# Kernel tuning notes

Measured on AMD Instinct MI355X. Metric: run time of the kernel, lower is better.

Reference implementation:

```python
import jax, jax.numpy as jnp
import numpy as np

N_EMBD = 1024
N_HEAD = 16
HEAD_SIZE = N_EMBD // N_HEAD
EPS = 1e-5


def layer_norm(x, gamma, beta):
    mu = jnp.mean(x, axis=-1, keepdims=True)
    var = jnp.var(x, axis=-1, keepdims=True)
    return (x - mu) * jax.lax.rsqrt(var + EPS) * gamma + beta


def setup_inputs() -> dict:
    key = jax.random.key(0)
    ks = jax.random.split(key, 12)
    B, T, C, H, hs = 2, 2048, N_EMBD, N_HEAD, HEAD_SIZE
    s = lambda fan_in: 1.0 / np.sqrt(fan_in)
    return {
        "x": jax.random.normal(ks[0], (B, T, C), dtype=jnp.float32),
        "Wq": jax.random.normal(ks[1], (H, C, hs), dtype=jnp.float32) * s(C),
        "Wk": jax.random.normal(ks[2], (H, C, hs), dtype=jnp.float32) * s(C),
        "Wv": jax.random.normal(ks[3], (H, C, hs), dtype=jnp.float32) * s(C),
        "Wproj": jax.random.normal(ks[4], (C, C), dtype=jnp.float32) * s(C),
        "bproj": jax.random.normal(ks[5], (C,), dtype=jnp.float32) * 0.01,
        "g1": jnp.ones((C,), dtype=jnp.float32),
        "b1": jnp.zeros((C,), dtype=jnp.float32),
        "g2": jnp.ones((C,), dtype=jnp.float32),
        "b2": jnp.zeros((C,), dtype=jnp.float32),
        "W_ff1": jax.random.normal(ks[6], (C, 4 * C), dtype=jnp.float32) * s(C),
        "b_ff1": jax.random.normal(ks[7], (4 * C,), dtype=jnp.float32) * 0.01,
        "W_ff2": jax.random.normal(ks[8], (4 * C, C), dtype=jnp.float32) * s(4 * C),
        "b_ff2": jax.random.normal(ks[9], (C,), dtype=jnp.float32) * 0.01,
    }


def reference(x, Wq, Wk, Wv, Wproj, bproj, g1, b1, g2, b2, W_ff1, b_ff1, W_ff2, b_ff2):
    B, T, C = x.shape
    # --- LN1 + multi-head causal self-attention ---
    h = layer_norm(x, g1, b1)
    q = jnp.einsum("btc,hcd->bhtd", h, Wq)  # [B,H,T,hs]
    k = jnp.einsum("btc,hcd->bhtd", h, Wk)
    v = jnp.einsum("btc,hcd->bhtd", h, Wv)
    scale = HEAD_SIZE ** -0.5
    wei = jnp.einsum("bhtd,bhsd->bhts", q, k) * scale  # [B,H,T,T]
    mask = jnp.tril(jnp.ones((T, T), dtype=bool))
    wei = jnp.where(mask, wei, -jnp.inf)
    wei = jax.nn.softmax(wei, axis=-1)
    out = jnp.einsum("bhts,bhsd->bhtd", wei, v)  # [B,H,T,hs]
    out = out.transpose(0, 2, 1, 3).reshape(B, T, C)  # concat heads
    sa = out @ Wproj + bproj
    x = x + sa
    # --- LN2 + FFN ---
    h2 = layer_norm(x, g2, b2)
    ff = jax.nn.relu(h2 @ W_ff1 + b_ff1) @ W_ff2 + b_ff2
    return x + ff
```

## Files before the change

### kernel.cpp

```cpp
#include <hip/hip_runtime.h>
#include <hip/hip_bf16.h>

#define N_EMBD 1024
#define N_HEAD 16
#define HEADSZ 64
#define BATCH  2
#define SEQ    2048
#define ROWS   (BATCH*SEQ)

typedef __attribute__((ext_vector_type(8))) short bf16x8;
typedef __attribute__((ext_vector_type(4))) float f32x4;

__device__ __forceinline__ short f2bs(float v){
    union { __hip_bfloat16 b; short s; } u; u.b = __float2bfloat16(v); return u.s;
}
__device__ __forceinline__ short scale8th(short s){
    union { unsigned i; float f; } u; u.i = ((unsigned)(unsigned short)s) << 16;
    return f2bs(u.f * 0.125f);
}
__device__ __forceinline__ void gload16(const short* g, short* l){
    __builtin_amdgcn_global_load_lds(
        (const __attribute__((address_space(1))) unsigned int*)g,
        (__attribute__((address_space(3))) unsigned int*)l, 16, 0, 0);
}

__global__ __launch_bounds__(256) void tr_cvt(const float* __restrict__ in,
                                              short* __restrict__ out,
                                              int R, int Cc,
                                              size_t in_z, size_t out_z)
{
    __shared__ float t[32][33];
    const int tx = threadIdx.x & 31, ty = threadIdx.x >> 5;
    const int j0 = blockIdx.x * 32, i0 = blockIdx.y * 32;
    const float* ip = in + (size_t)blockIdx.z * in_z;
    short* op = out + (size_t)blockIdx.z * out_z;
#pragma unroll
    for (int p = 0; p < 4; ++p)
        t[ty + p * 8][tx] = ip[(size_t)(i0 + ty + p * 8) * Cc + j0 + tx];
    __syncthreads();
#pragma unroll
    for (int p = 0; p < 4; ++p)
        op[(size_t)(j0 + ty + p * 8) * R + i0 + tx] = f2bs(t[tx][ty + p * 8]);
}

__global__ __launch_bounds__(256) void tr3_cvt(const float* __restrict__ Wq,
                                               const float* __restrict__ Wk,
                                               const float* __restrict__ Wv,
                                               short* __restrict__ w2t)
{
    __shared__ float t[32][33];
    const int tx = threadIdx.x & 31, ty = threadIdx.x >> 5;
    const int which = blockIdx.z >> 4, head = blockIdx.z & 15;
    const int j0 = blockIdx.x * 32, i0 = blockIdx.y * 32;
    const float* ip = (which == 0 ? Wq : which == 1 ? Wk : Wv) + (size_t)head * 65536;
    short* op = w2t + (size_t)which * 1048576 + (size_t)head * 65536;
#pragma unroll
    for (int p = 0; p < 4; ++p)
        t[ty + p * 8][tx] = ip[(size_t)(i0 + ty + p * 8) * 64 + j0 + tx];
    __syncthreads();
#pragma unroll
    for (int p = 0; p < 4; ++p)
        op[(size_t)(j0 + ty + p * 8) * 1024 + i0 + tx] = f2bs(t[tx][ty + p * 8]);
}

__global__ __launch_bounds__(256) void vt_tr(const short* __restrict__ qkv,
                                             short* __restrict__ vt)
{
    __shared__ short t[64][65];
    const int tid = threadIdx.x;
    const int sr = tid >> 2, sc = (tid & 3) * 16;
    const int col0 = blockIdx.x * 64, tok0 = blockIdx.y * 64;
    const short* ip = qkv + (size_t)(tok0 + sr) * 3072 + 2048 + col0 + sc;
    bf16x8 v0 = *(const bf16x8*)ip;
    bf16x8 v1 = *(const bf16x8*)(ip + 8);
#pragma unroll
    for (int i = 0; i < 8; ++i) { t[sr][sc + i] = v0[i]; t[sr][sc + 8 + i] = v1[i]; }
    __syncthreads();
    bf16x8 a, bq;
#pragma unroll
    for (int i = 0; i < 8; ++i) { a[i] = t[sc + i][sr]; bq[i] = t[sc + 8 + i][sr]; }
    short* op = vt + (size_t)(col0 + sr) * 4096 + tok0 + sc;
    *(bf16x8*)op = a;
    *(bf16x8*)(op + 8) = bq;
}

__global__ __launch_bounds__(256) void ln_k(const float* __restrict__ x,
                                            const float* __restrict__ g,
                                            const float* __restrict__ bta,
                                            short* __restrict__ out)
{
    const int row = blockIdx.x;
    const int tid = threadIdx.x;
    const float* xr = x + (size_t)row * N_EMBD;
    float4 v = *(const float4*)(xr + tid * 4);
    float s  = v.x + v.y + v.z + v.w;
    float s2 = v.x * v.x + v.y * v.y + v.z * v.z + v.w * v.w;
#pragma unroll
    for (int off = 32; off; off >>= 1) {
        s  += __shfl_xor(s,  off, 64);
        s2 += __shfl_xor(s2, off, 64);
    }
    __shared__ float rs[4], rs2[4];
    const int wave = tid >> 6, lane = tid & 63;
    if (lane == 0) { rs[wave] = s; rs2[wave] = s2; }
    __syncthreads();
    s  = rs[0] + rs[1] + rs[2] + rs[3];
    s2 = rs2[0] + rs2[1] + rs2[2] + rs2[3];
    const float mean = s * (1.f / N_EMBD);
    const float var  = s2 * (1.f / N_EMBD) - mean * mean;
    const float rsig = rsqrtf(var + 1e-5f);
    float4 gv = *(const float4*)(g + tid * 4);
    float4 bv = *(const float4*)(bta + tid * 4);
    short4 o;
    o.x = f2bs((v.x - mean) * rsig * gv.x + bv.x);
    o.y = f2bs((v.y - mean) * rsig * gv.y + bv.y);
    o.z = f2bs((v.z - mean) * rsig * gv.z + bv.z);
    o.w = f2bs((v.w - mean) * rsig * gv.w + bv.w);
    *(short4*)(out + (size_t)row * N_EMBD + tid * 4) = o;
}

__global__ __launch_bounds__(256) void pln_fin(const float* __restrict__ p0,
                                               const float* __restrict__ p1,
                                               const float* __restrict__ bias,
                                               const float* __restrict__ x,
                                               const float* __restrict__ g,
                                               const float* __restrict__ bta,
                                               float* __restrict__ x2,
                                               short* __restrict__ h2)
{
    const int row = blockIdx.x, tid = threadIdx.x;
    const size_t base = (size_t)row * N_EMBD + tid * 4;
    float4 a  = *(const float4*)(p0 + base);
    float4 c  = *(const float4*)(p1 + base);
    float4 xx = *(const float4*)(x + base);
    float4 bb = *(const float4*)(bias + tid * 4);
    float4 v;
    v.x = a.x + c.x + xx.x + bb.x;
    v.y = a.y + c.y + xx.y + bb.y;
    v.z = a.z + c.z + xx.z + bb.z;
    v.w = a.w + c.w + xx.w + bb.w;
    *(float4*)(x2 + base) = v;
    float s  = v.x + v.y + v.z + v.w;
    float s2 = v.x * v.x + v.y * v.y + v.z * v.z + v.w * v.w;
#pragma unroll
    for (int off = 32; off; off >>= 1) {
        s  += __shfl_xor(s,  off, 64);
        s2 += __shfl_xor(s2, off, 64);
    }
    __shared__ float rs[4], rs2[4];
    const int wave = tid >> 6, lane = tid & 63;
    if (lane == 0) { rs[wave] = s; rs2[wave] = s2; }
    __syncthreads();
    s  = rs[0] + rs[1] + rs[2] + rs[3];
    s2 = rs2[0] + rs2[1] + rs2[2] + rs2[3];
    const float mean = s * (1.f / N_EMBD);
    const float var  = s2 * (1.f / N_EMBD) - mean * mean;
    const float rsig = rsqrtf(var + 1e-5f);
    float4 gv = *(const float4*)(g + tid * 4);
    float4 bv = *(const float4*)(bta + tid * 4);
    short4 o;
    o.x = f2bs((v.x - mean) * rsig * gv.x + bv.x);
    o.y = f2bs((v.y - mean) * rsig * gv.y + bv.y);
    o.z = f2bs((v.z - mean) * rsig * gv.z + bv.z);
    o.w = f2bs((v.w - mean) * rsig * gv.w + bv.w);
    *(short4*)(h2 + base) = o;
}

__global__ __launch_bounds__(256) void mfma_gemm(
    const short* __restrict__ A,
    const short* __restrict__ Bt,
    const float* __restrict__ bias,
    const float* __restrict__ resid,
    float* __restrict__ outf,
    float* __restrict__ outf2,
    short* __restrict__ outb,
    int M, int N, int K, int kz, int relu)
{
    __shared__ __align__(16) short As[128 * 32];
    __shared__ __align__(16) short Bs[128 * 32];
    const int tid  = threadIdx.x;
    const int lane = tid & 63, w = tid >> 6;
    const int quad = lane >> 4, l16 = lane & 15;
    const int row0 = blockIdx.y * 128, col0 = blockIdx.x * 128;
    const int wm = (w >> 1) * 64, wn = (w & 1) * 64;
    const int koff = blockIdx.z * kz;
    const int kend = kz ? kz : K;

    f32x4 acc[4][4];
#pragma unroll
    for (int i = 0; i < 4; ++i)
#pragma unroll
        for (int j = 0; j < 4; ++j)
            acc[i][j] = f32x4{0.f, 0.f, 0.f, 0.f};

    const int c0  = w * 128 + lane;
    const int c1  = c0 + 64;
    const int ar0 = c0 >> 2, ak0 = (((c0 & 3) ^ ((ar0 >> 1) & 3))) * 8;
    const int ar1 = c1 >> 2, ak1 = (((c1 & 3) ^ ((ar1 >> 1) & 3))) * 8;
    const short* aG0 = A  + (size_t)(row0 + ar0) * K + koff + ak0;
    const short* aG1 = A  + (size_t)(row0 + ar1) * K + koff + ak1;
    const short* bG0 = Bt + (size_t)(col0 + ar0) * K + koff + ak0;
    const short* bG1 = Bt + (size_t)(col0 + ar1) * K + koff + ak1;
    short* aL0 = As + (size_t)w * 1024;
    short* aL1 = aL0 + 512;
    short* bL0 = Bs + (size_t)w * 1024;
    short* bL1 = bL0 + 512;

    const int gsw = (quad ^ ((l16 >> 1) & 3)) * 8;

    for (int k0 = 0; k0 < kend; k0 += 32) {
        __syncthreads();
        gload16(aG0 + k0, aL0);
        gload16(aG1 + k0, aL1);
        gload16(bG0 + k0, bL0);
        gload16(bG1 + k0, bL1);
        asm volatile("s_waitcnt vmcnt(0)" ::: "memory");
        __syncthreads();

        bf16x8 af[4], bfr[4];
#pragma unroll
        for (int i = 0; i < 4; ++i)
            af[i]  = *(const bf16x8*)(As + (wm + i * 16 + l16) * 32 + gsw);
#pragma unroll
        for (int j = 0; j < 4; ++j)
            bfr[j] = *(const bf16x8*)(Bs + (wn + j * 16 + l16) * 32 + gsw);
#pragma unroll
        for (int i = 0; i < 4; ++i)
#pragma unroll
            for (int j = 0; j < 4; ++j)
                acc[i][j] = __builtin_amdgcn_mfma_f32_16x16x32_bf16(
                    af[i], bfr[j], acc[i][j], 0, 0, 0);
    }

    float* of = blockIdx.z ? outf2 : outf;
#pragma unroll
    for (int i = 0; i < 4; ++i) {
        const int rbase = row0 + wm + i * 16 + quad * 4;
#pragma unroll
        for (int j = 0; j < 4; ++j) {
            const int c = col0 + wn + j * 16 + l16;
            const float bv = bias ? bias[c] : 0.f;
#pragma unroll
            for (int r = 0; r < 4; ++r) {
                float v = acc[i][j][r] + bv;
                if (relu) v = fmaxf(v, 0.f);
                const size_t idx = (size_t)(rbase + r) * N + c;
                if (resid) v += resid[idx];
                if (outb) outb[idx] = f2bs(v);
                else      of[idx] = v;
            }
        }
    }
}

__global__ __launch_bounds__(256) void mfma_gemm64(
    const short* __restrict__ A,
    const short* __restrict__ Bt,
    float* __restrict__ outf,
    float* __restrict__ outf2,
    int K, int kz)
{
    __shared__ __align__(16) short As[64 * 32];
    __shared__ __align__(16) short Bs[128 * 32];
    const int tid  = threadIdx.x;
    const int lane = tid & 63, w = tid >> 6;
    const int quad = lane >> 4, l16 = lane & 15;
    const int lin  = (int)blockIdx.y * 8 + (int)blockIdx.x;
    const int swz  = (lin & 7) * 64 + (lin >> 3);
    const int col0 = (swz & 7) * 128;
    const int row0 = (swz >> 3) * 64;
    const int wr = w >> 1, wc = w & 1;
    const int koff = blockIdx.z * kz;

    f32x4 acc[2][4];
#pragma unroll
    for (int i = 0; i < 2; ++i)
#pragma unroll
        for (int j = 0; j < 4; ++j)
            acc[i][j] = f32x4{0.f, 0.f, 0.f, 0.f};

    const int ia  = w * 64 + lane;
    const int ar  = ia >> 2;
    const int aak = ((ia & 3) ^ ((ar >> 1) & 3)) * 8;
    const short* aG = A + (size_t)(row0 + ar) * K + koff + aak;
    short* aL = As + w * 512;
    const int c0  = w * 128 + lane;
    const int c1  = c0 + 64;
    const int br0 = c0 >> 2, bk0 = ((c0 & 3) ^ ((br0 >> 1) & 3)) * 8;
    const int br1 = c1 >> 2, bk1 = ((c1 & 3) ^ ((br1 >> 1) & 3)) * 8;
    const short* bG0 = Bt + (size_t)(col0 + br0) * K + koff + bk0;
    const short* bG1 = Bt + (size_t)(col0 + br1) * K + koff + bk1;
    short* bL0 = Bs + (size_t)w * 1024;
    short* bL1 = bL0 + 512;

    const int gsw = (quad ^ ((l16 >> 1) & 3)) * 8;

    for (int k0 = 0; k0 < kz; k0 += 32) {
        __syncthreads();
        gload16(aG + k0, aL);
        gload16(bG0 + k0, bL0);
        gload16(bG1 + k0, bL1);
        asm volatile("s_waitcnt vmcnt(0)" ::: "memory");
        __syncthreads();

        bf16x8 af[2], bfr[4];
#pragma unroll
        for (int i = 0; i < 2; ++i)
            af[i]  = *(const bf16x8*)(As + (wr * 32 + i * 16 + l16) * 32 + gsw);
#pragma unroll
        for (int j = 0; j < 4; ++j)
            bfr[j] = *(const bf16x8*)(Bs + (wc * 64 + j * 16 + l16) * 32 + gsw);
#pragma unroll
        for (int i = 0; i < 2; ++i)
#pragma unroll
            for (int j = 0; j < 4; ++j)
                acc[i][j] = __builtin_amdgcn_mfma_f32_16x16x32_bf16(
                    af[i], bfr[j], acc[i][j], 0, 0, 0);
    }

    float* of = blockIdx.z ? outf2 : outf;
#pragma unroll
    for (int i = 0; i < 2; ++i) {
        const int rbase = row0 + wr * 32 + i * 16 + quad * 4;
#pragma unroll
        for (int j = 0; j < 4; ++j) {
            const int c = col0 + wc * 64 + j * 16 + l16;
#pragma unroll
            for (int r = 0; r < 4; ++r)
                of[(size_t)(rbase + r) * 1024 + c] = acc[i][j][r];
        }
    }
}

__global__ __launch_bounds__(256) void ff2_fin(const float* __restrict__ p0,
                                               const float* __restrict__ bias,
                                               const float* __restrict__ x2,
                                               float* __restrict__ out)
{
    const size_t i = ((size_t)blockIdx.x * 256 + threadIdx.x) * 4;
    float4 a = *(const float4*)(p0 + i);
    float4 b = *(const float4*)(out + i);
    float4 r = *(const float4*)(x2 + i);
    float4 bb = *(const float4*)(bias + (i & 1023));
    float4 o;
    o.x = a.x + b.x + r.x + bb.x;
    o.y = a.y + b.y + r.y + bb.y;
    o.z = a.z + b.z + r.z + bb.z;
    o.w = a.w + b.w + r.w + bb.w;
    *(float4*)(out + i) = o;
}

__global__ __launch_bounds__(256) void attn_k(const short* __restrict__ qkv,
                                              const short* __restrict__ vt,
                                              short* __restrict__ att)
{
    __shared__ __align__(16) short Ks[2][64 * 64];
    __shared__ __align__(16) short Vs[2][64 * 64];
    __shared__ __align__(16) short Ps[64 * 64];
    const int tid  = threadIdx.x;
    const int lane = tid & 63, w = tid >> 6;
    const int quad = lane >> 4, l16 = lane & 15;
    const int bh = blockIdx.y, b = bh >> 4, head = bh & 15;

    const int srow = lane >> 3;
    const int sw   = ((lane & 7) ^ srow) * 8;
    const int cidx = (quad ^ (l16 & 7)) * 8;

    const int k4 = (bh >> 3) & 3;
    int qt = (k4 & 2) ? ((int)blockIdx.x ^ 16) : (int)blockIdx.x;
    if (k4 & 1) qt = 31 - qt;
    const int t0 = qt * 64;
    const int ntiles = qt + 1;

    const short* qp = qkv + (size_t)(b * SEQ + t0 + w * 16 + l16) * 3072
                      + head * 64 + quad * 8;
    bf16x8 qf0 = *(const bf16x8*)qp;
    bf16x8 qf1 = *(const bf16x8*)(qp + 32);
#pragma unroll
    for (int i = 0; i < 8; ++i) { qf0[i] = scale8th(qf0[i]); qf1[i] = scale8th(qf1[i]); }

    float mrow = -INFINITY, lrow = 0.f;
    f32x4 O[4];
#pragma unroll
    for (int jn = 0; jn < 4; ++jn) O[jn] = f32x4{0.f, 0.f, 0.f, 0.f};

    {
        const short* kg = qkv + (size_t)(b * SEQ + w * 16 + srow) * 3072
                          + 1024 + head * 64 + sw;
        const short* vg = vt + (size_t)(head * 64 + w * 16 + srow) * 4096
                          + b * SEQ + sw;
        short* kL = Ks[0] + w * 1024;
        short* vL = Vs[0] + w * 1024;
        gload16(kg, kL); gload16(kg + (size_t)8 * 3072, kL + 512);
        gload16(vg, vL); gload16(vg + (size_t)8 * 4096, vL + 512);
    }

    for (int kt = 0; kt < ntiles; ++kt) {
        const int cur = kt & 1;
        asm volatile("s_waitcnt vmcnt(0) lgkmcnt(0)\n\ts_barrier" ::: "memory");
        if (kt + 1 < ntiles) {
            const int s1 = (kt + 1) * 64;
            const short* kg = qkv + (size_t)(b * SEQ + s1 + w * 16 + srow) * 3072
                              + 1024 + head * 64 + sw;
            const short* vg = vt + (size_t)(head * 64 + w * 16 + srow) * 4096
                              + b * SEQ + s1 + sw;
            short* kL = Ks[cur ^ 1] + w * 1024;
            short* vL = Vs[cur ^ 1] + w * 1024;
            gload16(kg, kL); gload16(kg + (size_t)8 * 3072, kL + 512);
            gload16(vg, vL); gload16(vg + (size_t)8 * 4096, vL + 512);
        }

        f32x4 S[4];
        const short* Kb = Ks[cur];
#pragma unroll
        for (int jn = 0; jn < 4; ++jn) {
            S[jn] = f32x4{0.f, 0.f, 0.f, 0.f};
            const short* kp = Kb + (jn * 16 + l16) * 64;
            bf16x8 b0 = *(const bf16x8*)(kp + cidx);
            bf16x8 b1 = *(const bf16x8*)(kp + (cidx ^ 32));
            S[jn] = __builtin_amdgcn_mfma_f32_16x16x32_bf16(b0, qf0, S[jn], 0, 0, 0);
            S[jn] = __builtin_amdgcn_mfma_f32_16x16x32_bf16(b1, qf1, S[jn], 0, 0, 0);
        }

        float Sv[4][4];
        const int qrow = t0 + w * 16 + l16;
        const int s0 = kt * 64;
#pragma unroll
        for (int jn = 0; jn < 4; ++jn)
#pragma unroll
            for (int r = 0; r < 4; ++r)
                Sv[jn][r] = S[jn][r];
        if (kt == ntiles - 1) {
#pragma unroll
            for (int jn = 0; jn < 4; ++jn)
#pragma unroll
                for (int r = 0; r < 4; ++r)
                    if (s0 + jn * 16 + quad * 4 + r > qrow) Sv[jn][r] = -INFINITY;
        }
        float tmx[4];
#pragma unroll
        for (int jn = 0; jn < 4; ++jn)
            tmx[jn] = fmaxf(fmaxf(Sv[jn][0], Sv[jn][1]), fmaxf(Sv[jn][2], Sv[jn][3]));
        float pm = fmaxf(fmaxf(tmx[0], tmx[1]), fmaxf(tmx[2], tmx[3]));
        pm = fmaxf(pm, __shfl_xor(pm, 16, 64));
        pm = fmaxf(pm, __shfl_xor(pm, 32, 64));
        const float mn    = fmaxf(mrow, pm);
        const float alpha = __expf(mrow - mn);
#pragma unroll
        for (int jn = 0; jn < 4; ++jn)
#pragma unroll
            for (int r = 0; r < 4; ++r)
                Sv[jn][r] = __expf(Sv[jn][r] - mn);
        float tsm[4];
#pragma unroll
        for (int jn = 0; jn < 4; ++jn)
            tsm[jn] = (Sv[jn][0] + Sv[jn][1]) + (Sv[jn][2] + Sv[jn][3]);
        float ps = (tsm[0] + tsm[1]) + (tsm[2] + tsm[3]);
        ps += __shfl_xor(ps, 16, 64);
        ps += __shfl_xor(ps, 32, 64);
        lrow = lrow * alpha + ps;
        mrow = mn;
#pragma unroll
        for (int r = 0; r < 4; ++r) {
            const float a = __shfl(alpha, quad * 4 + r, 64);
#pragma unroll
            for (int jn = 0; jn < 4; ++jn) O[jn][r] *= a;
        }

#pragma unroll
        for (int jn = 0; jn < 4; ++jn) {
            short4 pv;
            pv.x = f2bs(Sv[jn][0]); pv.y = f2bs(Sv[jn][1]);
            pv.z = f2bs(Sv[jn][2]); pv.w = f2bs(Sv[jn][3]);
            const int prow = w * 16 + l16;
            const int pcol = jn * 16 + quad * 4;
            const int chunk = (pcol >> 3) ^ (l16 & 7);
            *(short4*)(Ps + prow * 64 + chunk * 8 + (pcol & 7)) = pv;
        }
        asm volatile("s_waitcnt lgkmcnt(0)" ::: "memory");

        const short* pp = Ps + (w * 16 + l16) * 64;
        bf16x8 pf0 = *(const bf16x8*)(pp + cidx);
        bf16x8 pf1 = *(const bf16x8*)(pp + (cidx ^ 32));
        const short* Vb = Vs[cur];
#pragma unroll
        for (int jn = 0; jn < 4; ++jn) {
            const short* vp = Vb + (jn * 16 + l16) * 64;
            bf16x8 v0 = *(const bf16x8*)(vp + cidx);
            bf16x8 v1 = *(const bf16x8*)(vp + (cidx ^ 32));
            O[jn] = __builtin_amdgcn_mfma_f32_16x16x32_bf16(pf0, v0, O[jn], 0, 0, 0);
            O[jn] = __builtin_amdgcn_mfma_f32_16x16x32_bf16(pf1, v1, O[jn], 0, 0, 0);
        }
    }

#pragma unroll
    for (int r = 0; r < 4; ++r) {
        const float lr  = __shfl(lrow, quad * 4 + r, 64);
        const float inv = 1.f / lr;
        const size_t rowoff = (size_t)(b * SEQ + t0 + w * 16 + quad * 4 + r) * N_EMBD
                              + head * 64 + l16;
#pragma unroll
        for (int jn = 0; jn < 4; ++jn)
            att[rowoff + jn * 16] = f2bs(O[jn][r] * inv);
    }
}

extern "C" void kernel_launch(void* const* d_in, const int* in_sizes, int n_in,
                              void* d_out, int out_size, void* d_ws, size_t ws_size,
                              hipStream_t stream)
{
    const float* x     = (const float*)d_in[0];
    const float* Wq    = (const float*)d_in[1];
    const float* Wk    = (const float*)d_in[2];
    const float* Wv    = (const float*)d_in[3];
    const float* Wproj = (const float*)d_in[4];
    const float* bproj = (const float*)d_in[5];
    const float* g1    = (const float*)d_in[6];
    const float* b1    = (const float*)d_in[7];
    const float* g2    = (const float*)d_in[8];
    const float* b2    = (const float*)d_in[9];
    const float* Wff1  = (const float*)d_in[10];
    const float* bff1  = (const float*)d_in[11];
    const float* Wff2  = (const float*)d_in[12];
    const float* bff2  = (const float*)d_in[13];
    float* out = (float*)d_out;

    char* ws = (char*)d_ws;
    short* w2t  = (short*)(ws + 0);
    short* wpt  = (short*)(ws + 6291456);
    short* wf1t = (short*)(ws + 8388608);
    short* wf2t = (short*)(ws + 16777216);
    short* h    = (short*)(ws + 25165824);
    short* qkv  = (short*)(ws + 33554432);
    short* vt   = (short*)(ws + 58720256);
    short* att  = (short*)(ws + 67108864);
    float* x2   = (float*)(ws + 75497472);
    short* h2   = h;
    float* p0p  = (float*)(ws + 33554432);
    float* p1p  = (float*)(ws + 50331648);
    short* ff   = qkv;
    float* p0f  = (float*)(ws + 0);

    tr3_cvt<<<dim3(2, 32, 48),  256, 0, stream>>>(Wq, Wk, Wv, w2t);
    tr_cvt<<<dim3(32, 32, 1),  256, 0, stream>>>(Wproj, wpt,  1024, 1024, 0, 0);
    tr_cvt<<<dim3(128, 32, 1), 256, 0, stream>>>(Wff1, wf1t,  1024, 4096, 0, 0);
    tr_cvt<<<dim3(32, 128, 1), 256, 0, stream>>>(Wff2, wf2t,  4096, 1024, 0, 0);

    ln_k<<<ROWS, 256, 0, stream>>>(x, g1, b1, h);
    mfma_gemm<<<dim3(3072 / 128, ROWS / 128), 256, 0, stream>>>(
        h, w2t, nullptr, nullptr, nullptr, nullptr, qkv, ROWS, 3072, N_EMBD, 0, 0);
    vt_tr<<<dim3(16, 64), 256, 0, stream>>>(qkv, vt);
    attn_k<<<dim3(32, BATCH * N_HEAD), 256, 0, stream>>>(qkv, vt, att);
    mfma_gemm64<<<dim3(8, 64, 2), 256, 0, stream>>>(att, wpt, p0p, p1p, N_EMBD, 512);
    pln_fin<<<ROWS, 256, 0, stream>>>(p0p, p1p, bproj, x, g2, b2, x2, h2);
    mfma_gemm<<<dim3(4096 / 128, ROWS / 128), 256, 0, stream>>>(
        h2, wf1t, bff1, nullptr, nullptr, nullptr, ff, ROWS, 4096, N_EMBD, 0, 1);
    mfma_gemm64<<<dim3(8, 64, 2), 256, 0, stream>>>(ff, wf2t, p0f, out, 4096, 2048);
    ff2_fin<<<ROWS * N_EMBD / 1024, 256, 0, stream>>>(p0f, bff2, x2, out);
}
```

Baseline: 389.8 us.

## Double-buffer LDS tiles in MFMA GEMM kernels to overlap loads with compute

Both GEMM kernels now keep two LDS buffers for the A and B tiles and issue the global-to-LDS loads for the next K-step before computing on the current one. This replaces the old load-wait-compute sequence that had two barriers per iteration with a single wait and barrier after compute. The aim is to hide global memory latency behind the MFMA work. In exchange, LDS use per block doubles, which may reduce occupancy.

```diff
diff --git a/kernel.cpp b/kernel.cpp
--- a/kernel.cpp
+++ b/kernel.cpp
@@ -176,8 +176,8 @@
     short* __restrict__ outb,
     int M, int N, int K, int kz, int relu)
 {
-    __shared__ __align__(16) short As[128 * 32];
-    __shared__ __align__(16) short Bs[128 * 32];
+    __shared__ __align__(16) short As[2][128 * 32];
+    __shared__ __align__(16) short Bs[2][128 * 32];
     const int tid  = threadIdx.x;
     const int lane = tid & 63, w = tid >> 6;
     const int quad = lane >> 4, l16 = lane & 15;
@@ -201,35 +201,43 @@
     const short* aG1 = A  + (size_t)(row0 + ar1) * K + koff + ak1;
     const short* bG0 = Bt + (size_t)(col0 + ar0) * K + koff + ak0;
     const short* bG1 = Bt + (size_t)(col0 + ar1) * K + koff + ak1;
-    short* aL0 = As + (size_t)w * 1024;
-    short* aL1 = aL0 + 512;
-    short* bL0 = Bs + (size_t)w * 1024;
-    short* bL1 = bL0 + 512;
+    const int lofs = w * 1024;
 
     const int gsw = (quad ^ ((l16 >> 1) & 3)) * 8;
 
+    gload16(aG0, As[0] + lofs);
+    gload16(aG1, As[0] + lofs + 512);
+    gload16(bG0, Bs[0] + lofs);
+    gload16(bG1, Bs[0] + lofs + 512);
+    asm volatile("s_waitcnt vmcnt(0)" ::: "memory");
+    __syncthreads();
+
     for (int k0 = 0; k0 < kend; k0 += 32) {
-        __syncthreads();
-        gload16(aG0 + k0, aL0);
-        gload16(aG1 + k0, aL1);
-        gload16(bG0 + k0, bL0);
-        gload16(bG1 + k0, bL1);
-        asm volatile("s_waitcnt vmcnt(0)" ::: "memory");
-        __syncthreads();
+        const int cur = (k0 >> 5) & 1;
+        if (k0 + 32 < kend) {
+            const int nxt = cur ^ 1;
+            gload16(aG0 + k0 + 32, As[nxt] + lofs);
+            gload16(aG1 + k0 + 32, As[nxt] + lofs + 512);
+            gload16(bG0 + k0 + 32, Bs[nxt] + lofs);
+            gload16(bG1 + k0 + 32, Bs[nxt] + lofs + 512);
+        }
 
         bf16x8 af[4], bfr[4];
 #pragma unroll
         for (int i = 0; i < 4; ++i)
-            af[i]  = *(const bf16x8*)(As + (wm + i * 16 + l16) * 32 + gsw);
+            af[i]  = *(const bf16x8*)(As[cur] + (wm + i * 16 + l16) * 32 + gsw);
 #pragma unroll
         for (int j = 0; j < 4; ++j)
-            bfr[j] = *(const bf16x8*)(Bs + (wn + j * 16 + l16) * 32 + gsw);
+            bfr[j] = *(const bf16x8*)(Bs[cur] + (wn + j * 16 + l16) * 32 + gsw);
 #pragma unroll
         for (int i = 0; i < 4; ++i)
 #pragma unroll
             for (int j = 0; j < 4; ++j)
                 acc[i][j] = __builtin_amdgcn_mfma_f32_16x16x32_bf16(
                     af[i], bfr[j], acc[i][j], 0, 0, 0);
+
+        asm volatile("s_waitcnt vmcnt(0)" ::: "memory");
+        __syncthreads();
     }
 
     float* of = blockIdx.z ? outf2 : outf;
@@ -260,8 +268,8 @@
     float* __restrict__ outf2,
     int K, int kz)
 {
-    __shared__ __align__(16) short As[64 * 32];
-    __shared__ __align__(16) short Bs[128 * 32];
+    __shared__ __align__(16) short As[2][64 * 32];
+    __shared__ __align__(16) short Bs[2][128 * 32];
     const int tid  = threadIdx.x;
     const int lane = tid & 63, w = tid >> 6;
     const int quad = lane >> 4, l16 = lane & 15;
@@ -283,39 +291,48 @@
     const int ar  = ia >> 2;
     const int aak = ((ia & 3) ^ ((ar >> 1) & 3)) * 8;
     const short* aG = A + (size_t)(row0 + ar) * K + koff + aak;
-    short* aL = As + w * 512;
+    const int aofs = w * 512;
     const int c0  = w * 128 + lane;
     const int c1  = c0 + 64;
     const int br0 = c0 >> 2, bk0 = ((c0 & 3) ^ ((br0 >> 1) & 3)) * 8;
     const int br1 = c1 >> 2, bk1 = ((c1 & 3) ^ ((br1 >> 1) & 3)) * 8;
     const short* bG0 = Bt + (size_t)(col0 + br0) * K + koff + bk0;
     const short* bG1 = Bt + (size_t)(col0 + br1) * K + koff + bk1;
-    short* bL0 = Bs + (size_t)w * 1024;
-    short* bL1 = bL0 + 512;
+    const int bofs = w * 1024;
 
     const int gsw = (quad ^ ((l16 >> 1) & 3)) * 8;
 
+    gload16(aG, As[0] + aofs);
+    gload16(bG0, Bs[0] + bofs);
+    gload16(bG1, Bs[0] + bofs + 512);
+    asm volatile("s_waitcnt vmcnt(0)" ::: "memory");
+    __syncthreads();
+
     for (int k0 = 0; k0 < kz; k0 += 32) {
-        __syncthreads();
-        gload16(aG + k0, aL);
-        gload16(bG0 + k0, bL0);
-        gload16(bG1 + k0, bL1);
-        asm volatile("s_waitcnt vmcnt(0)" ::: "memory");
-        __syncthreads();
+        const int cur = (k0 >> 5) & 1;
+        if (k0 + 32 < kz) {
+            const int nxt = cur ^ 1;
+            gload16(aG + k0 + 32, As[nxt] + aofs);
+            gload16(bG0 + k0 + 32, Bs[nxt] + bofs);
+            gload16(bG1 + k0 + 32, Bs[nxt] + bofs + 512);
+        }
 
         bf16x8 af[2], bfr[4];
 #pragma unroll
         for (int i = 0; i < 2; ++i)
-            af[i]  = *(const bf16x8*)(As + (wr * 32 + i * 16 + l16) * 32 + gsw);
+            af[i]  = *(const bf16x8*)(As[cur] + (wr * 32 + i * 16 + l16) * 32 + gsw);
 #pragma unroll
         for (int j = 0; j < 4; ++j)
-            bfr[j] = *(const bf16x8*)(Bs + (wc * 64 + j * 16 + l16) * 32 + gsw);
+            bfr[j] = *(const bf16x8*)(Bs[cur] + (wc * 64 + j * 16 + l16) * 32 + gsw);
 #pragma unroll
         for (int i = 0; i < 2; ++i)
 #pragma unroll
             for (int j = 0; j < 4; ++j)
                 acc[i][j] = __builtin_amdgcn_mfma_f32_16x16x32_bf16(
                     af[i], bfr[j], acc[i][j], 0, 0, 0);
+
+        asm volatile("s_waitcnt vmcnt(0)" ::: "memory");
+        __syncthreads();
     }
 
     float* of = blockIdx.z ? outf2 : outf;
```

New measurement: 374.8 us. 3.8% less time.
